# Kernel optimization log

Measured on AMD Instinct MI355X. Metric: run time of the kernel, lower is better.

The kernel has to match this reference:

```python
import jax, jax.numpy as jnp
import numpy as np

N = 10000        # num_nodes
E = 320000       # num_edges
F_IN = 5         # nf_dim[0]
F_OUT = 64       # nf_dim[1]
EF = 2           # ef_dim
H = 1            # num_heads
C = 27           # GAT_dim
HID = 450        # hidden_dim
FIN = 128        # final_dim
MLP_H = 32       # hidden of edge MLP
NEG_SLOPE = 0.2  # GATConv leaky relu slope


def setup_inputs() -> dict:
    key = jax.random.key(0)
    ks = jax.random.split(key, 18)
    s = 0.05
    return {
        "x": jax.random.normal(ks[0], (N, F_IN), dtype=jnp.float32),
        "edge_index": jax.random.randint(ks[1], (2, E), 0, N),
        "edge_attr": jax.random.normal(ks[2], (E, EF), dtype=jnp.float32),
        # edge-conditioned MLP: Linear(EF,32) -> ReLU -> Linear(32, F_IN*F_OUT)
        "mlp_w1": jax.random.normal(ks[3], (EF, MLP_H), dtype=jnp.float32) * s,
        "mlp_b1": jnp.zeros((MLP_H,), dtype=jnp.float32),
        "mlp_w2": jax.random.normal(ks[4], (MLP_H, F_IN * F_OUT), dtype=jnp.float32) * s,
        "mlp_b2": jnp.zeros((F_IN * F_OUT,), dtype=jnp.float32),
        # NNConv root weight + bias
        "nn_root": jax.random.normal(ks[5], (F_IN, F_OUT), dtype=jnp.float32) * s,
        "nn_bias": jnp.zeros((F_OUT,), dtype=jnp.float32),
        # GATConv: linear [F_OUT -> H*C], attention vectors, bias
        "gat_w": jax.random.normal(ks[6], (F_OUT, H * C), dtype=jnp.float32) * s,
        "gat_att_src": jax.random.normal(ks[7], (H, C), dtype=jnp.float32) * s,
        "gat_att_dst": jax.random.normal(ks[8], (H, C), dtype=jnp.float32) * s,
        "gat_bias": jnp.zeros((H * C,), dtype=jnp.float32),
        # readout MLP
        "fc1_w": jax.random.normal(ks[9], (N * H * C, HID), dtype=jnp.float32) * 0.002,
        "fc1_b": jnp.zeros((HID,), dtype=jnp.float32),
        "fc2_w": jax.random.normal(ks[10], (HID, FIN), dtype=jnp.float32) * s,
        "fc2_b": jnp.zeros((FIN,), dtype=jnp.float32),
    }


def reference(x, edge_index, edge_attr, mlp_w1, mlp_b1, mlp_w2, mlp_b2,
              nn_root, nn_bias, gat_w, gat_att_src, gat_att_dst, gat_bias,
              fc1_w, fc1_b, fc2_w, fc2_b):
    src, dst = edge_index[0], edge_index[1]

    # ---- NNConv (edge-conditioned conv, aggr='add', with root weight) ----
    h = jax.nn.relu(edge_attr @ mlp_w1 + mlp_b1) @ mlp_w2 + mlp_b2    # [E, F_IN*F_OUT]
    w_e = h.reshape(E, F_IN, F_OUT)                                    # per-edge weight
    msg = jnp.einsum('ei,eio->eo', x[src], w_e)                        # [E, F_OUT]
    agg = jax.ops.segment_sum(msg, dst, num_segments=N)                # scatter-add at targets
    x1 = jax.nn.relu(agg + x @ nn_root + nn_bias)                      # [N, F_OUT]

    # ---- GATConv (heads=H, concat, add_self_loops=True) ----
    loop = jnp.arange(N, dtype=src.dtype)
    src2 = jnp.concatenate([src, loop])
    dst2 = jnp.concatenate([dst, loop])
    xl = (x1 @ gat_w).reshape(N, H, C)                                 # [N, H, C]
    a_src = jnp.einsum('nhc,hc->nh', xl, gat_att_src)                  # [N, H]
    a_dst = jnp.einsum('nhc,hc->nh', xl, gat_att_dst)
    alpha = jax.nn.leaky_relu(a_src[src2] + a_dst[dst2], NEG_SLOPE)    # [E2, H]
    # softmax over incoming edges of each target node (stable)
    amax = jax.ops.segment_max(alpha, dst2, num_segments=N)            # [N, H]
    ex = jnp.exp(alpha - amax[dst2])
    denom = jax.ops.segment_sum(ex, dst2, num_segments=N)              # [N, H]
    attn = ex / denom[dst2]                                            # [E2, H]
    out = jax.ops.segment_sum(attn[:, :, None] * xl[src2], dst2, num_segments=N)  # [N, H, C]
    x2 = jax.nn.relu(out.reshape(N, H * C) + gat_bias)                 # [N, H*C]

    # ---- readout MLP on flattened graph ----
    v = x2.reshape(-1)                                                 # [N*H*C]
    v = jax.nn.relu(v @ fc1_w + fc1_b)
    v = jax.nn.relu(v @ fc2_w + fc2_b)
    return v
```

## Files before the change

kernel.cpp:

```cpp
#include <hip/hip_runtime.h>

#define Nn 10000
#define Ee 320000
#define CC 27
#define NEG 0.2f
#define TOT 270000
#define HIDn 450
#define FINALn 128
#define FC1_ROWS 264

__global__ void k_deg(const int* __restrict__ ei, int* __restrict__ deg) {
    int e = blockIdx.x * blockDim.x + threadIdx.x;
    if (e < Ee) atomicAdd(&deg[ei[Ee + e]], 1);
}

__global__ __launch_bounds__(1024) void k_scan(const int* __restrict__ deg,
                                               int* __restrict__ off,
                                               int* __restrict__ cursor) {
    __shared__ int sums[1024];
    int tid = threadIdx.x;
    const int CH = 10;
    int start = tid * CH;
    int local[CH];
    int s = 0;
    #pragma unroll
    for (int i = 0; i < CH; ++i) {
        int idx = start + i;
        int v = (idx < Nn) ? deg[idx] : 0;
        local[i] = v; s += v;
    }
    sums[tid] = s;
    __syncthreads();
    for (int d = 1; d < 1024; d <<= 1) {
        int v = (tid >= d) ? sums[tid - d] : 0;
        __syncthreads();
        sums[tid] += v;
        __syncthreads();
    }
    int run = sums[tid] - s;
    #pragma unroll
    for (int i = 0; i < CH; ++i) {
        int idx = start + i;
        if (idx < Nn) { off[idx] = run; cursor[idx] = run; run += local[i]; }
    }
    if (tid == 1023) off[Nn] = sums[1023];
}

__global__ void k_scatter(const int* __restrict__ ei, int* __restrict__ cursor,
                          int* __restrict__ srcS, int* __restrict__ eidS) {
    int e = blockIdx.x * blockDim.x + threadIdx.x;
    if (e < Ee) {
        int d = ei[Ee + e];
        int p = atomicAdd(&cursor[d], 1);
        srcS[p] = ei[e];
        eidS[p] = e;
    }
}

__global__ __launch_bounds__(256) void k_msg(
    const float* __restrict__ x, const float* __restrict__ ea,
    const float* __restrict__ W1, const float* __restrict__ B1,
    const float* __restrict__ W2, const float* __restrict__ B2,
    const int* __restrict__ srcS, const int* __restrict__ eidS,
    float* __restrict__ msgbuf)
{
    int q = blockIdx.x * 256 + threadIdx.x;
    if (q >= Ee) return;
    int e = eidS[q];
    int s = srcS[q];
    float2 eav = *(const float2*)(ea + 2 * (size_t)e);
    float xs0 = x[s*5+0], xs1 = x[s*5+1], xs2 = x[s*5+2], xs3 = x[s*5+3], xs4 = x[s*5+4];

    float msg[64];
    #pragma unroll
    for (int o = 0; o < 64; ++o)
        msg[o] = xs0*B2[o] + xs1*B2[64+o] + xs2*B2[128+o] + xs3*B2[192+o] + xs4*B2[256+o];

    for (int k = 0; k < 32; ++k) {
        float hk = fmaxf(eav.x * W1[k] + eav.y * W1[32+k] + B1[k], 0.f);
        float t0 = hk*xs0, t1 = hk*xs1, t2 = hk*xs2, t3 = hk*xs3, t4 = hk*xs4;
        const float* __restrict__ w = W2 + k * 320;
        #pragma unroll
        for (int o = 0; o < 64; ++o)
            msg[o] += t0*w[o] + t1*w[64+o] + t2*w[128+o] + t3*w[192+o] + t4*w[256+o];
    }
    float4* mb = (float4*)(msgbuf + (size_t)q * 64);
    #pragma unroll
    for (int o4 = 0; o4 < 16; ++o4)
        mb[o4] = make_float4(msg[4*o4], msg[4*o4+1], msg[4*o4+2], msg[4*o4+3]);
}

__global__ __launch_bounds__(256) void k_nodeagg(
    const float* __restrict__ msgbuf, const int* __restrict__ off,
    const float* __restrict__ x, const float* __restrict__ nnroot,
    const float* __restrict__ nnbias, const float* __restrict__ gw,
    const float* __restrict__ attsrc, const float* __restrict__ attdst,
    float* __restrict__ xl, float* __restrict__ asrcA, float* __restrict__ adstA)
{
    int wave = threadIdx.x >> 6;
    int lane = threadIdx.x & 63;
    int n = blockIdx.x * 4 + wave;
    if (n >= Nn) return;
    int beg = off[n], end = off[n + 1];

    float aggv = 0.f;
    for (int j = beg; j < end; ++j) aggv += msgbuf[(size_t)j * 64 + lane];

    float xn0 = x[n*5+0], xn1 = x[n*5+1], xn2 = x[n*5+2], xn3 = x[n*5+3], xn4 = x[n*5+4];
    float v = aggv + nnbias[lane]
            + xn0*nnroot[lane] + xn1*nnroot[64+lane] + xn2*nnroot[128+lane]
            + xn3*nnroot[192+lane] + xn4*nnroot[256+lane];
    float x1v = fmaxf(v, 0.f);

    int c = (lane < CC) ? lane : 0;
    float xlc = 0.f;
    #pragma unroll
    for (int o = 0; o < 64; ++o) {
        float xo = __shfl(x1v, o);
        xlc += xo * gw[o * CC + c];
    }
    float as_ = (lane < CC) ? xlc * attsrc[c] : 0.f;
    float ad_ = (lane < CC) ? xlc * attdst[c] : 0.f;
    #pragma unroll
    for (int d = 1; d < 64; d <<= 1) {
        as_ += __shfl_xor(as_, d);
        ad_ += __shfl_xor(ad_, d);
    }
    if (lane < CC) xl[n * CC + lane] = xlc;
    if (lane == 0) { asrcA[n] = as_; adstA[n] = ad_; }
}

__global__ __launch_bounds__(256) void k_gat(
    const int* __restrict__ off, const int* __restrict__ srcS,
    const float* __restrict__ xl, const float* __restrict__ asrcA,
    const float* __restrict__ adstA, const float* __restrict__ gbias,
    float* __restrict__ x2f)
{
    int wave = threadIdx.x >> 6;
    int lane = threadIdx.x & 63;
    int n = blockIdx.x * 4 + wave;
    if (n >= Nn) return;
    int beg = off[n], end = off[n + 1];

    float adn = adstA[n];
    float aself = asrcA[n] + adn; aself = aself >= 0.f ? aself : NEG * aself;

    float m = aself;
    for (int j = beg + lane; j < end; j += 64) {
        float al = asrcA[srcS[j]] + adn; al = al >= 0.f ? al : NEG * al;
        m = fmaxf(m, al);
    }
    #pragma unroll
    for (int d = 1; d < 64; d <<= 1) m = fmaxf(m, __shfl_xor(m, d));

    int c = (lane < CC) ? lane : 0;
    float wself = __expf(aself - m);
    float denom = wself;
    float acc = wself * xl[n * CC + c];
    for (int j = beg; j < end; ++j) {
        int s = srcS[j];
        float al = asrcA[s] + adn; al = al >= 0.f ? al : NEG * al;
        float w = __expf(al - m);
        denom += w;
        acc += w * xl[s * CC + c];
    }
    if (lane < CC) {
        float r = acc / denom + gbias[c];
        x2f[n * CC + lane] = fmaxf(r, 0.f);
    }
}

__global__ __launch_bounds__(512) void k_fc1(
    const float* __restrict__ x2f, const float* __restrict__ fw,
    float* __restrict__ v1acc)
{
    int j = threadIdx.x;
    int t0 = blockIdx.x * FC1_ROWS;
    int t1 = t0 + FC1_ROWS; if (t1 > TOT) t1 = TOT;
    if (j >= HIDn) return;
    float acc = 0.f;
    for (int t = t0; t < t1; t += 4) {
        float4 sv = *(const float4*)(x2f + t);
        if (sv.x != 0.f) acc += sv.x * fw[(size_t)t       * HIDn + j];
        if (sv.y != 0.f) acc += sv.y * fw[(size_t)(t + 1) * HIDn + j];
        if (sv.z != 0.f) acc += sv.z * fw[(size_t)(t + 2) * HIDn + j];
        if (sv.w != 0.f) acc += sv.w * fw[(size_t)(t + 3) * HIDn + j];
    }
    atomicAdd(&v1acc[j], acc);
}

__global__ __launch_bounds__(1024) void k_fc2(
    const float* __restrict__ v1acc, const float* __restrict__ b1,
    const float* __restrict__ w2, const float* __restrict__ b2,
    float* __restrict__ out)
{
    __shared__ float red[1024];
    int tid = threadIdx.x;
    int j = tid & 127, c = tid >> 7;
    int i0 = c * 57;
    int i1 = i0 + 57; if (i1 > HIDn) i1 = HIDn;
    float acc = 0.f;
    for (int i = i0; i < i1; ++i) {
        float a = fmaxf(v1acc[i] + b1[i], 0.f);
        acc += a * w2[i * FINALn + j];
    }
    red[tid] = acc;
    __syncthreads();
    if (tid < FINALn) {
        float s = 0.f;
        #pragma unroll
        for (int c2 = 0; c2 < 8; ++c2) s += red[c2 * FINALn + tid];
        out[tid] = fmaxf(s + b2[tid], 0.f);
    }
}

extern "C" void kernel_launch(void* const* d_in, const int* in_sizes, int n_in,
                              void* d_out, int out_size, void* d_ws, size_t ws_size,
                              hipStream_t stream)
{
    const float* x      = (const float*)d_in[0];
    const int*   ei     = (const int*)  d_in[1];
    const float* ea     = (const float*)d_in[2];
    const float* mw1    = (const float*)d_in[3];
    const float* mb1    = (const float*)d_in[4];
    const float* mw2    = (const float*)d_in[5];
    const float* mb2    = (const float*)d_in[6];
    const float* nnroot = (const float*)d_in[7];
    const float* nnbias = (const float*)d_in[8];
    const float* gw     = (const float*)d_in[9];
    const float* atts   = (const float*)d_in[10];
    const float* attd   = (const float*)d_in[11];
    const float* gbias  = (const float*)d_in[12];
    const float* f1w    = (const float*)d_in[13];
    const float* f1b    = (const float*)d_in[14];
    const float* f2w    = (const float*)d_in[15];
    const float* f2b    = (const float*)d_in[16];
    float* out = (float*)d_out;

    char* ws = (char*)d_ws;
    size_t p = 0;
    auto alloc = [&](size_t bytes) -> char* {
        char* r = ws + p;
        p += (bytes + 255) & ~(size_t)255;
        return r;
    };
    float* msgbuf = (float*)alloc((size_t)Ee * 64 * 4);
    int*   deg    = (int*)  alloc(Nn * 4 + HIDn * 4);
    float* v1acc  = (float*)(deg + Nn);
    int*   off    = (int*)  alloc((Nn + 1) * 4);
    int*   cursor = (int*)  alloc(Nn * 4);
    int*   srcS   = (int*)  alloc(Ee * 4);
    int*   eidS   = (int*)  alloc(Ee * 4);
    float* xl     = (float*)alloc(Nn * CC * 4);
    float* asrcA  = (float*)alloc(Nn * 4);
    float* adstA  = (float*)alloc(Nn * 4);
    float* x2f    = (float*)alloc(Nn * CC * 4);

    hipMemsetAsync(deg, 0, Nn * 4 + HIDn * 4, stream);

    k_deg    <<<(Ee + 255) / 256, 256, 0, stream>>>(ei, deg);
    k_scan   <<<1, 1024, 0, stream>>>(deg, off, cursor);
    k_scatter<<<(Ee + 255) / 256, 256, 0, stream>>>(ei, cursor, srcS, eidS);
    k_msg    <<<Ee / 256, 256, 0, stream>>>(x, ea, mw1, mb1, mw2, mb2, srcS, eidS, msgbuf);
    k_nodeagg<<<(Nn + 3) / 4, 256, 0, stream>>>(msgbuf, off, x, nnroot, nnbias, gw, atts, attd,
                                                xl, asrcA, adstA);
    k_gat    <<<(Nn + 3) / 4, 256, 0, stream>>>(off, srcS, xl, asrcA, adstA, gbias, x2f);
    k_fc1    <<<(TOT + FC1_ROWS - 1) / FC1_ROWS, 512, 0, stream>>>(x2f, f1w, v1acc);
    k_fc2    <<<1, 1024, 0, stream>>>(v1acc, f1b, f2w, f2b, out);
}
```

Baseline: 917.4 us.

## Factor NNConv edge MLP through per-node aggregation and drop message buffer

The edge-conditioned message is linear in the second MLP layer, so each destination node now accumulates sum_e relu(h_k)*x_src and sum_e x_src over its incoming edges and applies W2 and B2 once per node. This replaces the per-edge 64-wide message computation and the 82 MB intermediate message buffer with small per-node reductions. The scatter pass packs source index and edge attributes into one float4 record for coalesced reads. The GAT aggregation also splits edges across two half-waves. Summation order changes, which can shift floating-point results slightly.

```diff
diff --git a/kernel.cpp b/kernel.cpp
--- a/kernel.cpp
+++ b/kernel.cpp
@@ -8,6 +8,8 @@
 #define HIDn 450
 #define FINALn 128
 #define FC1_ROWS 264
+
+__device__ __forceinline__ float lrelu(float v) { return v >= 0.f ? v : NEG * v; }
 
 __global__ void k_deg(const int* __restrict__ ei, int* __restrict__ deg) {
     int e = blockIdx.x * blockDim.x + threadIdx.x;
@@ -46,56 +48,90 @@
     if (tid == 1023) off[Nn] = sums[1023];
 }
 
-__global__ void k_scatter(const int* __restrict__ ei, int* __restrict__ cursor,
-                          int* __restrict__ srcS, int* __restrict__ eidS) {
+__global__ void k_scatter(const int* __restrict__ ei, const float* __restrict__ ea,
+                          int* __restrict__ cursor, float4* __restrict__ rec) {
     int e = blockIdx.x * blockDim.x + threadIdx.x;
     if (e < Ee) {
         int d = ei[Ee + e];
         int p = atomicAdd(&cursor[d], 1);
-        srcS[p] = ei[e];
-        eidS[p] = e;
-    }
-}
-
-__global__ __launch_bounds__(256) void k_msg(
-    const float* __restrict__ x, const float* __restrict__ ea,
+        float2 v = *(const float2*)(ea + 2 * (size_t)e);
+        rec[p] = make_float4(__int_as_float(ei[e]), v.x, v.y, 0.f);
+    }
+}
+
+__global__ __launch_bounds__(256) void k_agg(
+    const float4* __restrict__ rec, const int* __restrict__ off,
+    const float* __restrict__ x,
     const float* __restrict__ W1, const float* __restrict__ B1,
     const float* __restrict__ W2, const float* __restrict__ B2,
-    const int* __restrict__ srcS, const int* __restrict__ eidS,
-    float* __restrict__ msgbuf)
-{
-    int q = blockIdx.x * 256 + threadIdx.x;
-    if (q >= Ee) return;
-    int e = eidS[q];
-    int s = srcS[q];
-    float2 eav = *(const float2*)(ea + 2 * (size_t)e);
-    float xs0 = x[s*5+0], xs1 = x[s*5+1], xs2 = x[s*5+2], xs3 = x[s*5+3], xs4 = x[s*5+4];
-
-    float msg[64];
-    #pragma unroll
-    for (int o = 0; o < 64; ++o)
-        msg[o] = xs0*B2[o] + xs1*B2[64+o] + xs2*B2[128+o] + xs3*B2[192+o] + xs4*B2[256+o];
-
-    for (int k = 0; k < 32; ++k) {
-        float hk = fmaxf(eav.x * W1[k] + eav.y * W1[32+k] + B1[k], 0.f);
-        float t0 = hk*xs0, t1 = hk*xs1, t2 = hk*xs2, t3 = hk*xs3, t4 = hk*xs4;
-        const float* __restrict__ w = W2 + k * 320;
-        #pragma unroll
-        for (int o = 0; o < 64; ++o)
-            msg[o] += t0*w[o] + t1*w[64+o] + t2*w[128+o] + t3*w[192+o] + t4*w[256+o];
-    }
-    float4* mb = (float4*)(msgbuf + (size_t)q * 64);
-    #pragma unroll
-    for (int o4 = 0; o4 < 16; ++o4)
-        mb[o4] = make_float4(msg[4*o4], msg[4*o4+1], msg[4*o4+2], msg[4*o4+3]);
-}
-
-__global__ __launch_bounds__(256) void k_nodeagg(
-    const float* __restrict__ msgbuf, const int* __restrict__ off,
-    const float* __restrict__ x, const float* __restrict__ nnroot,
-    const float* __restrict__ nnbias, const float* __restrict__ gw,
-    const float* __restrict__ attsrc, const float* __restrict__ attdst,
+    const float* __restrict__ nnroot, const float* __restrict__ nnbias,
+    const float* __restrict__ gw, const float* __restrict__ attsrc,
+    const float* __restrict__ attdst,
     float* __restrict__ xl, float* __restrict__ asrcA, float* __restrict__ adstA)
+{
+    int wave = threadIdx.x >> 6;
+    int lane = threadIdx.x & 63;
+    int n = blockIdx.x * 4 + wave;
+    if (n >= Nn) return;
+    int k = lane & 31, half = lane >> 5;
+    float w1a = W1[k], w1b = W1[32 + k], b1k = B1[k];
+    int beg = off[n], end = off[n + 1];
+
+    float S0=0,S1=0,S2=0,S3=0,S4=0, T0=0,T1=0,T2=0,T3=0,T4=0;
+    for (int j = beg + half; j < end; j += 2) {
+        float4 r = rec[j];
+        int s = __float_as_int(r.x);
+        float h = fmaxf(r.y * w1a + r.z * w1b + b1k, 0.f);
+        const float* xp = x + 5 * (size_t)s;
+        float x0 = xp[0], x1 = xp[1], x2 = xp[2], x3 = xp[3], x4 = xp[4];
+        S0 += h * x0; S1 += h * x1; S2 += h * x2; S3 += h * x3; S4 += h * x4;
+        T0 += x0; T1 += x1; T2 += x2; T3 += x3; T4 += x4;
+    }
+    S0 += __shfl_xor(S0, 32); S1 += __shfl_xor(S1, 32); S2 += __shfl_xor(S2, 32);
+    S3 += __shfl_xor(S3, 32); S4 += __shfl_xor(S4, 32);
+    T0 += __shfl_xor(T0, 32); T1 += __shfl_xor(T1, 32); T2 += __shfl_xor(T2, 32);
+    T3 += __shfl_xor(T3, 32); T4 += __shfl_xor(T4, 32);
+
+    float agg = 0.f;
+    #pragma unroll
+    for (int kk = 0; kk < 32; ++kk) {
+        float s0 = __shfl(S0, kk), s1 = __shfl(S1, kk), s2 = __shfl(S2, kk);
+        float s3 = __shfl(S3, kk), s4 = __shfl(S4, kk);
+        const float* w = W2 + kk * 320;
+        agg += s0*w[lane] + s1*w[64+lane] + s2*w[128+lane] + s3*w[192+lane] + s4*w[256+lane];
+    }
+    agg += T0*B2[lane] + T1*B2[64+lane] + T2*B2[128+lane] + T3*B2[192+lane] + T4*B2[256+lane];
+
+    const float* xn = x + 5 * (size_t)n;
+    float xn0 = xn[0], xn1 = xn[1], xn2 = xn[2], xn3 = xn[3], xn4 = xn[4];
+    float v = agg + nnbias[lane]
+            + xn0*nnroot[lane] + xn1*nnroot[64+lane] + xn2*nnroot[128+lane]
+            + xn3*nnroot[192+lane] + xn4*nnroot[256+lane];
+    float x1v = fmaxf(v, 0.f);
+
+    int c = (lane < CC) ? lane : 0;
+    float xlc = 0.f;
+    #pragma unroll
+    for (int o = 0; o < 64; ++o) {
+        float xo = __shfl(x1v, o);
+        xlc += xo * gw[o * CC + c];
+    }
+    float as_ = (lane < CC) ? xlc * attsrc[c] : 0.f;
+    float ad_ = (lane < CC) ? xlc * attdst[c] : 0.f;
+    #pragma unroll
+    for (int d = 1; d < 64; d <<= 1) {
+        as_ += __shfl_xor(as_, d);
+        ad_ += __shfl_xor(ad_, d);
+    }
+    if (lane < CC) xl[n * CC + lane] = xlc;
+    if (lane == 0) { asrcA[n] = as_; adstA[n] = ad_; }
+}
+
+__global__ __launch_bounds__(256) void k_gat(
+    const int* __restrict__ off, const float4* __restrict__ rec,
+    const float* __restrict__ xl, const float* __restrict__ asrcA,
+    const float* __restrict__ adstA, const float* __restrict__ gbias,
+    float* __restrict__ x2f)
 {
     int wave = threadIdx.x >> 6;
     int lane = threadIdx.x & 63;
@@ -103,69 +139,34 @@
     if (n >= Nn) return;
     int beg = off[n], end = off[n + 1];
 
-    float aggv = 0.f;
-    for (int j = beg; j < end; ++j) aggv += msgbuf[(size_t)j * 64 + lane];
-
-    float xn0 = x[n*5+0], xn1 = x[n*5+1], xn2 = x[n*5+2], xn3 = x[n*5+3], xn4 = x[n*5+4];
-    float v = aggv + nnbias[lane]
-            + xn0*nnroot[lane] + xn1*nnroot[64+lane] + xn2*nnroot[128+lane]
-            + xn3*nnroot[192+lane] + xn4*nnroot[256+lane];
-    float x1v = fmaxf(v, 0.f);
-
-    int c = (lane < CC) ? lane : 0;
-    float xlc = 0.f;
-    #pragma unroll
-    for (int o = 0; o < 64; ++o) {
-        float xo = __shfl(x1v, o);
-        xlc += xo * gw[o * CC + c];
-    }
-    float as_ = (lane < CC) ? xlc * attsrc[c] : 0.f;
-    float ad_ = (lane < CC) ? xlc * attdst[c] : 0.f;
-    #pragma unroll
-    for (int d = 1; d < 64; d <<= 1) {
-        as_ += __shfl_xor(as_, d);
-        ad_ += __shfl_xor(ad_, d);
-    }
-    if (lane < CC) xl[n * CC + lane] = xlc;
-    if (lane == 0) { asrcA[n] = as_; adstA[n] = ad_; }
-}
-
-__global__ __launch_bounds__(256) void k_gat(
-    const int* __restrict__ off, const int* __restrict__ srcS,
-    const float* __restrict__ xl, const float* __restrict__ asrcA,
-    const float* __restrict__ adstA, const float* __restrict__ gbias,
-    float* __restrict__ x2f)
-{
-    int wave = threadIdx.x >> 6;
-    int lane = threadIdx.x & 63;
-    int n = blockIdx.x * 4 + wave;
-    if (n >= Nn) return;
-    int beg = off[n], end = off[n + 1];
-
     float adn = adstA[n];
-    float aself = asrcA[n] + adn; aself = aself >= 0.f ? aself : NEG * aself;
+    float aself = lrelu(asrcA[n] + adn);
 
     float m = aself;
     for (int j = beg + lane; j < end; j += 64) {
-        float al = asrcA[srcS[j]] + adn; al = al >= 0.f ? al : NEG * al;
-        m = fmaxf(m, al);
+        int s = __float_as_int(rec[j].x);
+        m = fmaxf(m, lrelu(asrcA[s] + adn));
     }
     #pragma unroll
     for (int d = 1; d < 64; d <<= 1) m = fmaxf(m, __shfl_xor(m, d));
 
-    int c = (lane < CC) ? lane : 0;
+    int half = lane >> 5;
+    int c = lane & 31; int cc = (c < CC) ? c : 0;
+    float denom = 0.f, acc = 0.f;
+    for (int j = beg + half; j < end; j += 2) {
+        int s = __float_as_int(rec[j].x);
+        float w = __expf(lrelu(asrcA[s] + adn) - m);
+        denom += w;
+        acc += w * xl[s * CC + cc];
+    }
+    denom += __shfl_xor(denom, 32);
+    acc   += __shfl_xor(acc, 32);
     float wself = __expf(aself - m);
-    float denom = wself;
-    float acc = wself * xl[n * CC + c];
-    for (int j = beg; j < end; ++j) {
-        int s = srcS[j];
-        float al = asrcA[s] + adn; al = al >= 0.f ? al : NEG * al;
-        float w = __expf(al - m);
-        denom += w;
-        acc += w * xl[s * CC + c];
-    }
+    denom += wself;
+    acc   += wself * xl[n * CC + cc];
+
     if (lane < CC) {
-        float r = acc / denom + gbias[c];
+        float r = acc / denom + gbias[lane];
         x2f[n * CC + lane] = fmaxf(r, 0.f);
     }
 }
@@ -244,27 +245,25 @@
         p += (bytes + 255) & ~(size_t)255;
         return r;
     };
-    float* msgbuf = (float*)alloc((size_t)Ee * 64 * 4);
-    int*   deg    = (int*)  alloc(Nn * 4 + HIDn * 4);
-    float* v1acc  = (float*)(deg + Nn);
-    int*   off    = (int*)  alloc((Nn + 1) * 4);
-    int*   cursor = (int*)  alloc(Nn * 4);
-    int*   srcS   = (int*)  alloc(Ee * 4);
-    int*   eidS   = (int*)  alloc(Ee * 4);
-    float* xl     = (float*)alloc(Nn * CC * 4);
-    float* asrcA  = (float*)alloc(Nn * 4);
-    float* adstA  = (float*)alloc(Nn * 4);
-    float* x2f    = (float*)alloc(Nn * CC * 4);
+    float4* rec   = (float4*)alloc((size_t)Ee * 16);
+    int*    deg   = (int*)   alloc(Nn * 4 + HIDn * 4);
+    float*  v1acc = (float*)(deg + Nn);
+    int*    off   = (int*)   alloc((Nn + 1) * 4);
+    int*    cursor= (int*)   alloc(Nn * 4);
+    float*  xl    = (float*) alloc(Nn * CC * 4);
+    float*  asrcA = (float*) alloc(Nn * 4);
+    float*  adstA = (float*) alloc(Nn * 4);
+    float*  x2f   = (float*) alloc(TOT * 4);
 
     hipMemsetAsync(deg, 0, Nn * 4 + HIDn * 4, stream);
 
     k_deg    <<<(Ee + 255) / 256, 256, 0, stream>>>(ei, deg);
     k_scan   <<<1, 1024, 0, stream>>>(deg, off, cursor);
-    k_scatter<<<(Ee + 255) / 256, 256, 0, stream>>>(ei, cursor, srcS, eidS);
-    k_msg    <<<Ee / 256, 256, 0, stream>>>(x, ea, mw1, mb1, mw2, mb2, srcS, eidS, msgbuf);
-    k_nodeagg<<<(Nn + 3) / 4, 256, 0, stream>>>(msgbuf, off, x, nnroot, nnbias, gw, atts, attd,
+    k_scatter<<<(Ee + 255) / 256, 256, 0, stream>>>(ei, ea, cursor, rec);
+    k_agg    <<<(Nn + 3) / 4, 256, 0, stream>>>(rec, off, x, mw1, mb1, mw2, mb2,
+                                                nnroot, nnbias, gw, atts, attd,
                                                 xl, asrcA, adstA);
-    k_gat    <<<(Nn + 3) / 4, 256, 0, stream>>>(off, srcS, xl, asrcA, adstA, gbias, x2f);
+    k_gat    <<<(Nn + 3) / 4, 256, 0, stream>>>(off, rec, xl, asrcA, adstA, gbias, x2f);
     k_fc1    <<<(TOT + FC1_ROWS - 1) / FC1_ROWS, 512, 0, stream>>>(x2f, f1w, v1acc);
     k_fc2    <<<1, 1024, 0, stream>>>(v1acc, f1b, f2w, f2b, out);
 }
```

Result: faster. 788.3 us (-14.1%).
